# Optimization experiments

Measured on AMD Instinct MI355X. Metric: run time of the kernel, lower is better.

## Reference

```python
import jax, jax.numpy as jnp
import numpy as np

B, H, L, D = 2, 16, 2048, 64


def setup_inputs() -> dict:
    key = jax.random.key(0)
    kq, kk, kv = jax.random.split(key, 3)
    return {
        "query": jax.random.normal(kq, (B, H, L, D), dtype=jnp.float32),
        "key": jax.random.normal(kk, (B, H, L, D), dtype=jnp.float32),
        "value": jax.random.normal(kv, (B, H, L, D), dtype=jnp.float32),
        "dhead": D,
        "causal": 1,
    }


def reference(query, key, value, dhead, causal):
    # mode='dhead': muP attention with scale 1/dhead (not 1/sqrt(dhead)).
    # Inputs/outputs in [B, H, L, D] layout (the torch code transposes to
    # [B, L, H, D] for the einsum and transposes back; net layout is the same).
    scale = 1.0 / dhead
    a = jnp.einsum('bhld,bhLd->bhlL', query, key) * scale  # [B,H,L,L]
    if causal:
        seq = a.shape[-1]
        mask = jnp.tril(jnp.ones((seq, seq), dtype=bool))  # [L,L]
        a = jnp.where(mask, a, jnp.float32(-jnp.inf))
    a = jax.nn.softmax(a, axis=-1)
    out = jnp.einsum('bhlL,bhLd->bhld', a, value)  # [B,H,L,D]
    return out
```

## Files before the change

kernel.cpp:

```cpp
#include <hip/hip_runtime.h>

#define BHH 32
#define SEQ 2048
#define DH 64
#define BQ 64
#define BK 64
#define NKT (SEQ / BK)
#define NQB (SEQ / BQ)
#define NT  (BHH * NKT)

typedef __attribute__((ext_vector_type(8))) _Float16 half8_t;
typedef __attribute__((ext_vector_type(4))) _Float16 half4_t;
typedef __attribute__((ext_vector_type(4))) float f32x4;

__device__ __forceinline__ void async_copy16(const void* g, const void* lds) {
    __builtin_amdgcn_global_load_lds(
        (const __attribute__((address_space(1))) unsigned int*)g,
        (__attribute__((address_space(3))) unsigned int*)lds, 16, 0, 0);
}

__global__ __launch_bounds__(256) void prep_kv(const float* __restrict__ K,
                                               const float* __restrict__ V,
                                               _Float16* __restrict__ Kf,
                                               _Float16* __restrict__ Vf) {
    __shared__ _Float16 l[64 * 76];
    const int t = threadIdx.x;
    const int wave = t >> 6, lane = t & 63, ln15 = lane & 15, quad = lane >> 4;
    const int row = t >> 2, col0 = (t & 3) * 16;
    int b = blockIdx.x;

    if (b < NT) {
        const float4* src = (const float4*)(K + (size_t)b * 4096 + row * 64 + col0);
        #pragma unroll
        for (int q = 0; q < 2; ++q) {
            float4 f0 = src[q * 2], f1 = src[q * 2 + 1];
            half8_t w = { (_Float16)f0.x, (_Float16)f0.y, (_Float16)f0.z, (_Float16)f0.w,
                          (_Float16)f1.x, (_Float16)f1.y, (_Float16)f1.z, (_Float16)f1.w };
            *(half8_t*)&l[row * 72 + col0 + q * 8] = w;
        }
        __syncthreads();
        #pragma unroll
        for (int p = 0; p < 2; ++p) {
            const int bid = wave * 2 + p, c = bid >> 1, k0 = bid & 1;
            half8_t w = *(const half8_t*)&l[(c * 16 + ln15) * 72 + k0 * 32 + quad * 8];
            *(half8_t*)&Kf[(size_t)b * 4096 + bid * 512 + lane * 8] = w;
        }
    } else {
        b -= NT;
        const float4* src = (const float4*)(V + (size_t)b * 4096 + row * 64 + col0);
        #pragma unroll
        for (int q = 0; q < 4; ++q) {
            float4 f = src[q];
            half4_t w = { (_Float16)f.x, (_Float16)f.y, (_Float16)f.z, (_Float16)f.w };
            *(half4_t*)&l[row * 76 + col0 + q * 4] = w;
        }
        __syncthreads();
        #pragma unroll
        for (int p = 0; p < 4; ++p) {
            const int f = wave * 4 + p, cn = f >> 2, c = f & 3;
            half4_t w;
            #pragma unroll
            for (int j = 0; j < 4; ++j)
                w[j] = l[(c * 16 + quad * 4 + j) * 76 + cn * 16 + ln15];
            *(half4_t*)&Vf[(size_t)b * 4096 + f * 256 + lane * 4] = w;
        }
    }
}

__global__ __launch_bounds__(256) void fattn_kernel(
        const float* __restrict__ Q, const _Float16* __restrict__ Kf,
        const _Float16* __restrict__ Vf, float* __restrict__ O) {
    const int bh = blockIdx.x & 31;
    const int r = blockIdx.x >> 5, j = r & 7, rnd = r >> 3;
    const int qb = (rnd == 0) ? 31 - j : (rnd == 1) ? 16 + j
                 : (rnd == 2) ? 15 - j : j;
    const int tid  = threadIdx.x;
    const int wave = tid >> 6;
    const int lane = tid & 63;
    const int ln15 = lane & 15;
    const int quad = lane >> 4;

    __shared__ _Float16 ldsK[2][4096];
    __shared__ _Float16 ldsV[2][4096];

    const size_t base = (size_t)bh * SEQ * DH;
    const int q0   = qb * BQ;
    const int qrow = q0 + wave * 16;

    const float qscale = 1.44269504f / 64.0f;
    half8_t qfrag[2];
    {
        const float* qp = Q + base + (size_t)(qrow + ln15) * DH + quad * 8;
        #pragma unroll
        for (int k0 = 0; k0 < 2; ++k0) {
            float4 a = *(const float4*)(qp + k0 * 32);
            float4 b = *(const float4*)(qp + k0 * 32 + 4);
            qfrag[k0] = (half8_t){
                (_Float16)(a.x * qscale), (_Float16)(a.y * qscale),
                (_Float16)(a.z * qscale), (_Float16)(a.w * qscale),
                (_Float16)(b.x * qscale), (_Float16)(b.y * qscale),
                (_Float16)(b.z * qscale), (_Float16)(b.w * qscale) };
        }
    }

    f32x4 acc[4] = {};
    float l_i = 0.f;
    const size_t tb = (size_t)(bh * NKT) * 4096;

    #define STAGE(kt_, b_) do {                                              \
        const size_t toff = tb + (size_t)(kt_) * 4096;                       \
        _Pragma("unroll")                                                    \
        for (int i_ = 0; i_ < 4; ++i_) {                                     \
            const int bid_ = wave * 4 + i_;                                  \
            if (bid_ < 8)                                                    \
                async_copy16(Kf + toff + bid_ * 512 + lane * 8,              \
                             &ldsK[b_][bid_ * 512]);                         \
            else                                                             \
                async_copy16(Vf + toff + (bid_ - 8) * 512 + lane * 8,        \
                             &ldsV[b_][(bid_ - 8) * 512]);                   \
        }                                                                    \
    } while (0)

    const int nkt = qb + 1;
    STAGE(0, 0);
    __syncthreads();

    for (int kt = 0; kt < nkt; ++kt) {
        const _Float16* kvk = ldsK[kt & 1];
        const _Float16* kvv = ldsV[kt & 1];
        if (kt + 1 < nkt) STAGE(kt + 1, (kt + 1) & 1);

        f32x4 st[4];
        #pragma unroll
        for (int c = 0; c < 4; ++c) {
            half8_t kf0 = *(const half8_t*)&kvk[(c * 2 + 0) * 512 + lane * 8];
            half8_t kf1 = *(const half8_t*)&kvk[(c * 2 + 1) * 512 + lane * 8];
            f32x4 a = {};
            a = __builtin_amdgcn_mfma_f32_16x16x32_f16(kf0, qfrag[0], a, 0, 0, 0);
            a = __builtin_amdgcn_mfma_f32_16x16x32_f16(kf1, qfrag[1], a, 0, 0, 0);
            st[c] = a;
        }

        const int kbase = kt * BK;
        const bool needmask = (kt == qb);
        const int rowi = qrow + ln15;
        half4_t pfrag[4];
        float psum = 0.f;
        #pragma unroll
        for (int c = 0; c < 4; ++c) {
            #pragma unroll
            for (int rr = 0; rr < 4; ++rr) {
                float v = __builtin_amdgcn_exp2f(st[c][rr]);
                if (needmask && (kbase + c * 16 + quad * 4 + rr) > rowi) v = 0.f;
                pfrag[c][rr] = (_Float16)v;
                psum += v;
            }
        }
        psum += __shfl_xor(psum, 16);
        psum += __shfl_xor(psum, 32);
        l_i += psum;

        #pragma unroll
        for (int cn = 0; cn < 4; ++cn) {
            #pragma unroll
            for (int c = 0; c < 4; ++c) {
                half4_t vf = *(const half4_t*)&kvv[(cn * 4 + c) * 256 + lane * 4];
                acc[cn] = __builtin_amdgcn_mfma_f32_16x16x16f16(vf, pfrag[c], acc[cn], 0, 0, 0);
            }
        }
        __syncthreads();
    }

    {
        const float rl = 1.0f / l_i;
        float* op = O + base + (size_t)(qrow + ln15) * DH;
        #pragma unroll
        for (int cn = 0; cn < 4; ++cn) {
            float4 o;
            o.x = acc[cn][0] * rl;
            o.y = acc[cn][1] * rl;
            o.z = acc[cn][2] * rl;
            o.w = acc[cn][3] * rl;
            *(float4*)(op + cn * 16 + quad * 4) = o;
        }
    }
    #undef STAGE
}

extern "C" void kernel_launch(void* const* d_in, const int* in_sizes, int n_in,
                              void* d_out, int out_size, void* d_ws, size_t ws_size,
                              hipStream_t stream) {
    const float* Q = (const float*)d_in[0];
    const float* K = (const float*)d_in[1];
    const float* V = (const float*)d_in[2];
    float* O = (float*)d_out;
    _Float16* Kf = (_Float16*)d_ws;
    _Float16* Vf = Kf + (size_t)NT * 4096;
    prep_kv<<<2 * NT, 256, 0, stream>>>(K, V, Kf, Vf);
    fattn_kernel<<<NQB * BHH, 256, 0, stream>>>(Q, Kf, Vf, O);
}
```

Baseline: 129.2 us.

## Use 16x16x32 MFMA for PV with repacked V layout and deferred row-sum reduction

Repacks V in the prep kernel into 8-half fragments so the P·V product uses eight 16x16x32 f16 MFMAs per tile instead of sixteen 16x16x16 ones, with P packed through cvt_pkrtz. The per-iteration cross-lane shuffles for the softmax denominator are moved to a single reduction after the loop, and the mask is applied only on the diagonal tile. KV staging addresses are precomputed per wave, the first tile's load is issued before the Q load, and launch bounds request 4 blocks per CU. This cuts MFMA issue count and per-iteration ALU/shuffle work, but changes the fragment layout both kernels must agree on and uses round-toward-zero conversion for P.

```diff
diff --git a/kernel.cpp b/kernel.cpp
--- a/kernel.cpp
+++ b/kernel.cpp
@@ -11,12 +11,17 @@
 
 typedef __attribute__((ext_vector_type(8))) _Float16 half8_t;
 typedef __attribute__((ext_vector_type(4))) _Float16 half4_t;
+typedef __attribute__((ext_vector_type(2))) _Float16 half2_t;
 typedef __attribute__((ext_vector_type(4))) float f32x4;
 
 __device__ __forceinline__ void async_copy16(const void* g, const void* lds) {
     __builtin_amdgcn_global_load_lds(
         (const __attribute__((address_space(1))) unsigned int*)g,
         (__attribute__((address_space(3))) unsigned int*)lds, 16, 0, 0);
+}
+
+__device__ __forceinline__ half2_t pkrtz(float a, float b) {
+    return __builtin_bit_cast(half2_t, __builtin_amdgcn_cvt_pkrtz(a, b));
 }
 
 __global__ __launch_bounds__(256) void prep_kv(const float* __restrict__ K,
@@ -56,18 +61,20 @@
         }
         __syncthreads();
         #pragma unroll
-        for (int p = 0; p < 4; ++p) {
-            const int f = wave * 4 + p, cn = f >> 2, c = f & 3;
-            half4_t w;
+        for (int p = 0; p < 2; ++p) {
+            const int f = wave * 2 + p, cn = f >> 1, k1 = f & 1;
+            half8_t w;
             #pragma unroll
-            for (int j = 0; j < 4; ++j)
-                w[j] = l[(c * 16 + quad * 4 + j) * 76 + cn * 16 + ln15];
-            *(half4_t*)&Vf[(size_t)b * 4096 + f * 256 + lane * 4] = w;
-        }
-    }
-}
-
-__global__ __launch_bounds__(256) void fattn_kernel(
+            for (int jj = 0; jj < 8; ++jj) {
+                const int krow = k1 * 32 + ((jj & 4) << 2) + quad * 4 + (jj & 3);
+                w[jj] = l[krow * 76 + cn * 16 + ln15];
+            }
+            *(half8_t*)&Vf[(size_t)b * 4096 + f * 512 + lane * 8] = w;
+        }
+    }
+}
+
+__global__ __launch_bounds__(256, 4) void fattn_kernel(
         const float* __restrict__ Q, const _Float16* __restrict__ Kf,
         const _Float16* __restrict__ Vf, float* __restrict__ O) {
     const int bh = blockIdx.x & 31;
@@ -86,6 +93,21 @@
     const size_t base = (size_t)bh * SEQ * DH;
     const int q0   = qb * BQ;
     const int qrow = q0 + wave * 16;
+    const size_t tb = (size_t)(bh * NKT) * 4096;
+
+    const _Float16* gsrc = ((wave < 2) ? Kf : Vf) + tb + (wave & 1) * 2048 + lane * 8;
+    _Float16* dstA = ((wave < 2) ? &ldsK[0][0] : &ldsV[0][0]) + (wave & 1) * 2048;
+    _Float16* dstB = ((wave < 2) ? &ldsK[1][0] : &ldsV[1][0]) + (wave & 1) * 2048;
+
+    #define STAGE(kt_, d_) do {                                          \
+        const _Float16* s_ = gsrc + (size_t)(kt_) * 4096;                \
+        _Float16* dd_ = (d_);                                            \
+        _Pragma("unroll")                                                \
+        for (int i_ = 0; i_ < 4; ++i_)                                   \
+            async_copy16(s_ + i_ * 512, dd_ + i_ * 512);                 \
+    } while (0)
+
+    STAGE(0, dstA);
 
     const float qscale = 1.44269504f / 64.0f;
     half8_t qfrag[2];
@@ -94,84 +116,89 @@
         #pragma unroll
         for (int k0 = 0; k0 < 2; ++k0) {
             float4 a = *(const float4*)(qp + k0 * 32);
-            float4 b = *(const float4*)(qp + k0 * 32 + 4);
+            float4 b2 = *(const float4*)(qp + k0 * 32 + 4);
             qfrag[k0] = (half8_t){
                 (_Float16)(a.x * qscale), (_Float16)(a.y * qscale),
                 (_Float16)(a.z * qscale), (_Float16)(a.w * qscale),
-                (_Float16)(b.x * qscale), (_Float16)(b.y * qscale),
-                (_Float16)(b.z * qscale), (_Float16)(b.w * qscale) };
+                (_Float16)(b2.x * qscale), (_Float16)(b2.y * qscale),
+                (_Float16)(b2.z * qscale), (_Float16)(b2.w * qscale) };
         }
     }
 
     f32x4 acc[4] = {};
-    float l_i = 0.f;
-    const size_t tb = (size_t)(bh * NKT) * 4096;
-
-    #define STAGE(kt_, b_) do {                                              \
-        const size_t toff = tb + (size_t)(kt_) * 4096;                       \
-        _Pragma("unroll")                                                    \
-        for (int i_ = 0; i_ < 4; ++i_) {                                     \
-            const int bid_ = wave * 4 + i_;                                  \
-            if (bid_ < 8)                                                    \
-                async_copy16(Kf + toff + bid_ * 512 + lane * 8,              \
-                             &ldsK[b_][bid_ * 512]);                         \
-            else                                                             \
-                async_copy16(Vf + toff + (bid_ - 8) * 512 + lane * 8,        \
-                             &ldsV[b_][(bid_ - 8) * 512]);                   \
-        }                                                                    \
-    } while (0)
-
-    const int nkt = qb + 1;
-    STAGE(0, 0);
+    float l_lane = 0.f;
+
+    const _Float16* kA = &ldsK[0][0] + lane * 8;
+    const _Float16* kB = &ldsK[1][0] + lane * 8;
+    const _Float16* vA = &ldsV[0][0] + lane * 8;
+    const _Float16* vB = &ldsV[1][0] + lane * 8;
+    const int myrel = wave * 16 + ln15;
+    const int kq4 = quad * 4;
+
     __syncthreads();
 
-    for (int kt = 0; kt < nkt; ++kt) {
-        const _Float16* kvk = ldsK[kt & 1];
-        const _Float16* kvv = ldsV[kt & 1];
-        if (kt + 1 < nkt) STAGE(kt + 1, (kt + 1) & 1);
+    for (int kt = 0; kt <= qb; ++kt) {
+        const _Float16* kk = (kt & 1) ? kB : kA;
+        const _Float16* vv = (kt & 1) ? vB : vA;
+        if (kt < qb) STAGE(kt + 1, ((kt + 1) & 1) ? dstB : dstA);
 
         f32x4 st[4];
         #pragma unroll
         for (int c = 0; c < 4; ++c) {
-            half8_t kf0 = *(const half8_t*)&kvk[(c * 2 + 0) * 512 + lane * 8];
-            half8_t kf1 = *(const half8_t*)&kvk[(c * 2 + 1) * 512 + lane * 8];
+            half8_t kf0 = *(const half8_t*)(kk + c * 1024);
+            half8_t kf1 = *(const half8_t*)(kk + c * 1024 + 512);
             f32x4 a = {};
             a = __builtin_amdgcn_mfma_f32_16x16x32_f16(kf0, qfrag[0], a, 0, 0, 0);
             a = __builtin_amdgcn_mfma_f32_16x16x32_f16(kf1, qfrag[1], a, 0, 0, 0);
             st[c] = a;
         }
 
-        const int kbase = kt * BK;
-        const bool needmask = (kt == qb);
-        const int rowi = qrow + ln15;
-        half4_t pfrag[4];
-        float psum = 0.f;
-        #pragma unroll
-        for (int c = 0; c < 4; ++c) {
+        float p[4][4];
+        #pragma unroll
+        for (int c = 0; c < 4; ++c)
             #pragma unroll
-            for (int rr = 0; rr < 4; ++rr) {
-                float v = __builtin_amdgcn_exp2f(st[c][rr]);
-                if (needmask && (kbase + c * 16 + quad * 4 + rr) > rowi) v = 0.f;
-                pfrag[c][rr] = (_Float16)v;
-                psum += v;
-            }
-        }
-        psum += __shfl_xor(psum, 16);
-        psum += __shfl_xor(psum, 32);
-        l_i += psum;
+            for (int rr = 0; rr < 4; ++rr)
+                p[c][rr] = __builtin_amdgcn_exp2f(st[c][rr]);
+
+        if (kt == qb) {
+            #pragma unroll
+            for (int c = 0; c < 4; ++c)
+                #pragma unroll
+                for (int rr = 0; rr < 4; ++rr)
+                    if (c * 16 + kq4 + rr > myrel) p[c][rr] = 0.f;
+        }
+
+        float s0 = (p[0][0] + p[0][1]) + (p[0][2] + p[0][3]);
+        float s1 = (p[1][0] + p[1][1]) + (p[1][2] + p[1][3]);
+        float s2 = (p[2][0] + p[2][1]) + (p[2][2] + p[2][3]);
+        float s3 = (p[3][0] + p[3][1]) + (p[3][2] + p[3][3]);
+        l_lane += (s0 + s1) + (s2 + s3);
+
+        union P8 { half2_t h2[4]; half8_t h8; };
+        P8 u0, u1;
+        u0.h2[0] = pkrtz(p[0][0], p[0][1]);
+        u0.h2[1] = pkrtz(p[0][2], p[0][3]);
+        u0.h2[2] = pkrtz(p[1][0], p[1][1]);
+        u0.h2[3] = pkrtz(p[1][2], p[1][3]);
+        u1.h2[0] = pkrtz(p[2][0], p[2][1]);
+        u1.h2[1] = pkrtz(p[2][2], p[2][3]);
+        u1.h2[2] = pkrtz(p[3][0], p[3][1]);
+        u1.h2[3] = pkrtz(p[3][2], p[3][3]);
+        half8_t pb0 = u0.h8, pb1 = u1.h8;
 
         #pragma unroll
         for (int cn = 0; cn < 4; ++cn) {
-            #pragma unroll
-            for (int c = 0; c < 4; ++c) {
-                half4_t vf = *(const half4_t*)&kvv[(cn * 4 + c) * 256 + lane * 4];
-                acc[cn] = __builtin_amdgcn_mfma_f32_16x16x16f16(vf, pfrag[c], acc[cn], 0, 0, 0);
-            }
+            half8_t vf0 = *(const half8_t*)(vv + cn * 1024);
+            acc[cn] = __builtin_amdgcn_mfma_f32_16x16x32_f16(vf0, pb0, acc[cn], 0, 0, 0);
+            half8_t vf1 = *(const half8_t*)(vv + cn * 1024 + 512);
+            acc[cn] = __builtin_amdgcn_mfma_f32_16x16x32_f16(vf1, pb1, acc[cn], 0, 0, 0);
         }
         __syncthreads();
     }
 
     {
+        float l_i = l_lane + __shfl_xor(l_lane, 16);
+        l_i += __shfl_xor(l_i, 32);
         const float rl = 1.0f / l_i;
         float* op = O + base + (size_t)(qrow + ln15) * DH;
         #pragma unroll
@@ -181,7 +208,7 @@
             o.y = acc[cn][1] * rl;
             o.z = acc[cn][2] * rl;
             o.w = acc[cn][3] * rl;
-            *(float4*)(op + cn * 16 + quad * 4) = o;
+            *(float4*)(op + cn * 16 + kq4) = o;
         }
     }
     #undef STAGE
```

Measured after the change: 121.9 us. -5.6%, faster.
